# Optimization experiments

Measured on AMD Instinct MI355X. Metric: run time of the kernel, lower is better.

Reference implementation:

```python
import jax, jax.numpy as jnp
import numpy as np

D_MODEL = 1024
N_HEADS = 16
D_HEAD = D_MODEL // N_HEADS  # 64
SCALE = 1.0 / float(np.sqrt(D_HEAD))


def setup_inputs() -> dict:
    key = jax.random.key(0)
    kx, kq, kk, kv, ko = jax.random.split(key, 5)
    B, L = 1, 4096
    x = jax.random.normal(kx, (B, L, D_MODEL), dtype=jnp.float32)
    init = 0.02  # small init so softmax isn't saturated
    Wq = jax.random.normal(kq, (D_MODEL, D_MODEL), dtype=jnp.float32) * init
    Wk = jax.random.normal(kk, (D_MODEL, D_MODEL), dtype=jnp.float32) * init
    Wv = jax.random.normal(kv, (D_MODEL, D_MODEL), dtype=jnp.float32) * init
    Wo = jax.random.normal(ko, (D_MODEL, D_MODEL), dtype=jnp.float32) * init
    return {"x": x, "Wq": Wq, "Wk": Wk, "Wv": Wv, "Wo": Wo}


def reference(x, Wq, Wk, Wv, Wo):
    # x: [B, L, d_model]; torch Linear (no bias): y = x @ W.T
    B, L, _ = x.shape

    def split_heads(t):  # [B, L, d_model] -> [B, H, L, Dh]
        return t.reshape(B, L, N_HEADS, D_HEAD).transpose(0, 2, 1, 3)

    q = split_heads(x @ Wq.T)
    k = split_heads(x @ Wk.T)
    v = split_heads(x @ Wv.T)

    # Full (non-flash) attention: explicit [B, H, L, L] scores (causal=False, eval dropout=0)
    scores = jnp.einsum("bhld,bhmd->bhlm", q, k) * SCALE
    attn = jax.nn.softmax(scores, axis=-1)
    out = jnp.einsum("bhlm,bhmd->bhld", attn, v)

    out = out.transpose(0, 2, 1, 3).reshape(B, L, D_MODEL)
    return out @ Wo.T
```

## Files before the change

kernel.cpp:

```cpp
#include <hip/hip_runtime.h>

typedef _Float16 f16_t;
typedef __fp16 fp16x2 __attribute__((ext_vector_type(2)));
typedef _Float16 f16x2 __attribute__((ext_vector_type(2)));
typedef _Float16 f16x4 __attribute__((ext_vector_type(4)));
typedef _Float16 f16x8 __attribute__((ext_vector_type(8)));
typedef float f32x4 __attribute__((ext_vector_type(4)));

#define D_MODEL 1024
#define LSEQ 4096
#define NH 16
#define DH 64
#define QSCALE 0.18033688011112042f

#define GLDS16(g, l)                                                     \
    __builtin_amdgcn_global_load_lds(                                    \
        (const __attribute__((address_space(1))) void*)(g),              \
        (__attribute__((address_space(3))) void*)(l), 16, 0, 0)

#define WAIT_VM(n) asm volatile("s_waitcnt vmcnt(" #n ")" ::: "memory")

__global__ __launch_bounds__(256) void cvt_x(const float* __restrict__ in,
                                             f16_t* __restrict__ out, int n) {
    int i = (blockIdx.x * 256 + threadIdx.x) * 4;
    if (i + 3 < n) {
        float4 v = *(const float4*)&in[i];
        alignas(8) f16_t o4[4] = {(f16_t)v.x, (f16_t)v.y, (f16_t)v.z, (f16_t)v.w};
        *(uint2*)&out[i] = *(const uint2*)o4;
    }
}

__global__ __launch_bounds__(256) void cvt_w4(const float* __restrict__ w0,
                                              const float* __restrict__ w1,
                                              const float* __restrict__ w2,
                                              const float* __restrict__ w3,
                                              f16_t* __restrict__ out) {
    const int q = blockIdx.y;
    const float* src = (q == 0) ? w0 : (q == 1) ? w1 : (q == 2) ? w2 : w3;
    const float scale = (q == 0) ? QSCALE : 1.f;
    int i = (blockIdx.x * 256 + threadIdx.x) * 4;
    float4 v = *(const float4*)&src[i];
    alignas(8) f16_t o4[4] = {(f16_t)(v.x * scale), (f16_t)(v.y * scale),
                              (f16_t)(v.z * scale), (f16_t)(v.w * scale)};
    *(uint2*)&out[(size_t)q * (D_MODEL * D_MODEL) + i] = *(const uint2*)o4;
}

__global__ __launch_bounds__(256, 3) void gemm_f16(const f16_t* __restrict__ A,
                                                   const f16_t* __restrict__ B,
                                                   void* __restrict__ Cout,
                                                   int M, int N, int K, int mode) {
    __shared__ alignas(16) f16_t As[3][128 * 32];
    __shared__ alignas(16) f16_t Bs[3][128 * 32];

    const int tid  = threadIdx.x;
    const int wave = tid >> 6;
    const int lane = tid & 63;
    const int quad = lane >> 4;
    const int l16  = lane & 15;
    const int wm = (wave & 1) * 64;
    const int wn = (wave >> 1) * 64;
    const int bm = blockIdx.x * 128;
    const int bn = blockIdx.y * 128;

    f32x4 acc[4][4] = {};
    const int nk = K / 32;

    auto stage = [&](int kt, int b) {
        const int c0 = wave * 2;
        GLDS16(&A[(size_t)(bm + c0 * 16 + l16) * K + kt * 32 + quad * 8],
               &As[b][c0 * 512]);
        GLDS16(&A[(size_t)(bm + (c0 + 1) * 16 + l16) * K + kt * 32 + quad * 8],
               &As[b][(c0 + 1) * 512]);
        GLDS16(&B[(size_t)(bn + c0 * 16 + l16) * K + kt * 32 + quad * 8],
               &Bs[b][c0 * 512]);
        GLDS16(&B[(size_t)(bn + (c0 + 1) * 16 + l16) * K + kt * 32 + quad * 8],
               &Bs[b][(c0 + 1) * 512]);
    };

    stage(0, 0);
    stage(1, 1);
    for (int kt = 0; kt < nk; ++kt) {
        const int cb = kt % 3;
        if (kt < nk - 1) WAIT_VM(4);
        else             WAIT_VM(0);
        __syncthreads();
        if (kt + 2 < nk) stage(kt + 2, (kt + 2) % 3);

        f16x8 af[4], bfr[4];
#pragma unroll
        for (int mt = 0; mt < 4; ++mt)
            af[mt] = *(const f16x8*)&As[cb][((wm >> 4) + mt) * 512 + lane * 8];
#pragma unroll
        for (int nt = 0; nt < 4; ++nt)
            bfr[nt] = *(const f16x8*)&Bs[cb][((wn >> 4) + nt) * 512 + lane * 8];
#pragma unroll
        for (int mt = 0; mt < 4; ++mt)
#pragma unroll
            for (int nt = 0; nt < 4; ++nt)
                acc[mt][nt] = __builtin_amdgcn_mfma_f32_16x16x32_f16(
                    bfr[nt], af[mt], acc[mt][nt], 0, 0, 0);
    }

#pragma unroll
    for (int mt = 0; mt < 4; ++mt)
#pragma unroll
        for (int nt = 0; nt < 4; ++nt) {
            int row = bm + wm + mt * 16 + l16;
            int col = bn + wn + nt * 16 + quad * 4;
            if (mode == 0) {
                f16x4 p = {(f16_t)acc[mt][nt][0], (f16_t)acc[mt][nt][1],
                           (f16_t)acc[mt][nt][2], (f16_t)acc[mt][nt][3]};
                *(f16x4*)&((f16_t*)Cout)[((size_t)(col >> 6) * M + row) * 64 +
                                         (col & 63)] = p;
            } else {
                *(f32x4*)&((float*)Cout)[(size_t)row * N + col] = acc[mt][nt];
            }
        }
}

__global__ __launch_bounds__(256) void transpose_v(const f16_t* __restrict__ vh,
                                                   f16_t* __restrict__ v4) {
    __shared__ f16_t Ts[64][72];
    const int t = threadIdx.x;
    const int lt = blockIdx.x;
    const int head = blockIdx.y;

#pragma unroll
    for (int i = 0; i < 2; ++i) {
        int idx = t + i * 256;
        int row = idx >> 3, part = idx & 7;
        *(uint4*)&Ts[row][part * 8] =
            *(const uint4*)&vh[((size_t)head * LSEQ + lt * 64 + row) * DH + part * 8];
    }
    __syncthreads();

    const int c8  = t >> 5;
    const int mtp = c8 >> 2, dt = c8 & 3;
    const int l0  = (t & 31) * 2;
    alignas(16) f16_t buf[16];
#pragma unroll
    for (int li = 0; li < 2; ++li) {
        const int l = l0 + li;
        const int g = l >> 4, l16 = l & 15;
#pragma unroll
        for (int j = 0; j < 8; ++j) {
            int key = mtp * 32 + (j < 4 ? 4 * g + j : 16 + 4 * g + (j - 4));
            buf[li * 8 + j] = Ts[key][dt * 16 + l16];
        }
    }
    f16_t* dst = v4 + (size_t)head * (LSEQ * DH) + (size_t)lt * 4096 + c8 * 512 + l0 * 8;
    *(uint4*)&dst[0] = *(const uint4*)&buf[0];
    *(uint4*)&dst[8] = *(const uint4*)&buf[8];
}

__global__ __launch_bounds__(512, 4) void attn_kernel(const f16_t* __restrict__ qh,
                                                      const f16_t* __restrict__ kh,
                                                      const f16_t* __restrict__ v4,
                                                      f16_t* __restrict__ ao) {
    __shared__ alignas(16) f16_t smem[32768];
    __shared__ alignas(16) float lscr[8 * 64];
    f16_t* KsB = smem;
    f16_t* VsB = smem + 16384;

    const int tid  = threadIdx.x;
    const int wave = tid >> 6;
    const int lane = tid & 63;
    const int quad = lane >> 4;
    const int l16  = lane & 15;
    const int wq   = wave & 3;
    const int kha  = wave >> 2;

    const int id = blockIdx.x;
    const int head = id & 15;
    const int qrow0 = (id >> 4) * 128 + wq * 32;

    const f16_t* Q  = qh + (size_t)head * LSEQ * DH;
    const f16_t* K  = kh + (size_t)head * LSEQ * DH;
    const f16_t* V4 = v4 + (size_t)head * (LSEQ * DH);

    f16x8 qf[2][2];
#pragma unroll
    for (int qt = 0; qt < 2; ++qt)
#pragma unroll
        for (int kc = 0; kc < 2; ++kc)
            qf[qt][kc] = *(const f16x8*)
                &Q[(size_t)(qrow0 + qt * 16 + l16) * DH + kc * 32 + quad * 8];

    f32x4 o[4][2] = {};
    float lp[2] = {0.f, 0.f};

    auto stage = [&](int kt, int b) {
        f16_t* ks = KsB + (kha * 2 + b) * 4096;
        f16_t* vs = VsB + (kha * 2 + b) * 4096;
        const int ktg = kha * 32 + kt;
#pragma unroll
        for (int jj = 0; jj < 2; ++jj) {
            const int j = wq * 2 + jj;
            GLDS16(&K[(size_t)(ktg * 64 + wq * 16 + l16) * DH + jj * 32 + quad * 8],
                   &ks[j * 512]);
            GLDS16(&V4[(size_t)ktg * 4096 + wq * 1024 + jj * 512 + lane * 8],
                   &vs[wq * 1024 + jj * 512]);
        }
    };

    const int NT = LSEQ / 2 / 64;
    stage(0, 0);
    for (int kt = 0; kt < NT; ++kt) {
        const int cb = kt & 1;
        WAIT_VM(0);
        __syncthreads();
        if (kt + 1 < NT) stage(kt + 1, cb ^ 1);

        const f16_t* ks = KsB + (kha * 2 + cb) * 4096;
        const f16_t* vs = VsB + (kha * 2 + cb) * 4096;

#pragma unroll
        for (int mtp = 0; mtp < 2; ++mtp) {
            f32x4 s[2][2] = {};
#pragma unroll
            for (int h = 0; h < 2; ++h) {
                const int mt = mtp * 2 + h;
                f16x8 kf0 = *(const f16x8*)&ks[(mt * 2 + 0) * 512 + lane * 8];
                f16x8 kf1 = *(const f16x8*)&ks[(mt * 2 + 1) * 512 + lane * 8];
#pragma unroll
                for (int qt = 0; qt < 2; ++qt) {
                    s[h][qt] = __builtin_amdgcn_mfma_f32_16x16x32_f16(
                        kf0, qf[qt][0], s[h][qt], 0, 0, 0);
                    s[h][qt] = __builtin_amdgcn_mfma_f32_16x16x32_f16(
                        kf1, qf[qt][1], s[h][qt], 0, 0, 0);
                }
            }

            f16x8 vfd[4];
#pragma unroll
            for (int dt = 0; dt < 4; ++dt)
                vfd[dt] = *(const f16x8*)&vs[(mtp * 4 + dt) * 512 + lane * 8];

#pragma unroll
            for (int qt = 0; qt < 2; ++qt) {
                float e0 = __builtin_amdgcn_exp2f(s[0][qt][0]);
                float e1 = __builtin_amdgcn_exp2f(s[0][qt][1]);
                float e2 = __builtin_amdgcn_exp2f(s[0][qt][2]);
                float e3 = __builtin_amdgcn_exp2f(s[0][qt][3]);
                float e4 = __builtin_amdgcn_exp2f(s[1][qt][0]);
                float e5 = __builtin_amdgcn_exp2f(s[1][qt][1]);
                float e6 = __builtin_amdgcn_exp2f(s[1][qt][2]);
                float e7 = __builtin_amdgcn_exp2f(s[1][qt][3]);
                lp[qt] += ((e0 + e1) + (e2 + e3)) + ((e4 + e5) + (e6 + e7));
                fp16x2 p01 = __builtin_amdgcn_cvt_pkrtz(e0, e1);
                fp16x2 p23 = __builtin_amdgcn_cvt_pkrtz(e2, e3);
                fp16x2 p45 = __builtin_amdgcn_cvt_pkrtz(e4, e5);
                fp16x2 p67 = __builtin_amdgcn_cvt_pkrtz(e6, e7);
                f16x8 p = {__builtin_bit_cast(f16x2, p01)[0],
                           __builtin_bit_cast(f16x2, p01)[1],
                           __builtin_bit_cast(f16x2, p23)[0],
                           __builtin_bit_cast(f16x2, p23)[1],
                           __builtin_bit_cast(f16x2, p45)[0],
                           __builtin_bit_cast(f16x2, p45)[1],
                           __builtin_bit_cast(f16x2, p67)[0],
                           __builtin_bit_cast(f16x2, p67)[1]};
#pragma unroll
                for (int dt = 0; dt < 4; ++dt)
                    o[dt][qt] = __builtin_amdgcn_mfma_f32_16x16x32_f16(
                        vfd[dt], p, o[dt][qt], 0, 0, 0);
            }
        }
    }

    __syncthreads();
    float* scr = (float*)smem;
    if (wave >= 4) {
#pragma unroll
        for (int dt = 0; dt < 4; ++dt)
#pragma unroll
            for (int qt = 0; qt < 2; ++qt)
                *(f32x4*)&scr[(((wave - 4) * 8 + dt * 2 + qt) * 64 + lane) * 4] =
                    o[dt][qt];
#pragma unroll
        for (int qt = 0; qt < 2; ++qt)
            lscr[((wave - 4) * 2 + qt) * 64 + lane] = lp[qt];
    }
    __syncthreads();
    if (wave < 4) {
#pragma unroll
        for (int dt = 0; dt < 4; ++dt)
#pragma unroll
            for (int qt = 0; qt < 2; ++qt)
                o[dt][qt] += *(const f32x4*)
                    &scr[((wave * 8 + dt * 2 + qt) * 64 + lane) * 4];
#pragma unroll
        for (int qt = 0; qt < 2; ++qt) {
            float t = lp[qt] + lscr[(wave * 2 + qt) * 64 + lane];
            t += __shfl_xor(t, 16, 64);
            t += __shfl_xor(t, 32, 64);
            lp[qt] = 1.f / t;
        }
#pragma unroll
        for (int dt = 0; dt < 4; ++dt)
#pragma unroll
            for (int qt = 0; qt < 2; ++qt) {
                f16x4 ov = {(f16_t)(o[dt][qt][0] * lp[qt]),
                            (f16_t)(o[dt][qt][1] * lp[qt]),
                            (f16_t)(o[dt][qt][2] * lp[qt]),
                            (f16_t)(o[dt][qt][3] * lp[qt])};
                int qrow = qrow0 + qt * 16 + l16;
                *(f16x4*)&ao[(size_t)qrow * D_MODEL + head * 64 + dt * 16 +
                             quad * 4] = ov;
            }
    }
}

extern "C" void kernel_launch(void* const* d_in, const int* in_sizes, int n_in,
                              void* d_out, int out_size, void* d_ws, size_t ws_size,
                              hipStream_t stream) {
    const float* x  = (const float*)d_in[0];
    const float* Wq = (const float*)d_in[1];
    const float* Wk = (const float*)d_in[2];
    const float* Wv = (const float*)d_in[3];
    const float* Wo = (const float*)d_in[4];

    f16_t* xb = (f16_t*)d_ws;
    f16_t* wq = xb + (size_t)LSEQ * D_MODEL;
    f16_t* wo = wq + (size_t)3 * D_MODEL * D_MODEL;
    f16_t* qh = wo + (size_t)D_MODEL * D_MODEL;
    f16_t* kh = qh + (size_t)LSEQ * D_MODEL;
    f16_t* vh = kh + (size_t)LSEQ * D_MODEL;
    f16_t* v4 = vh + (size_t)LSEQ * D_MODEL;
    f16_t* ao = v4 + (size_t)LSEQ * D_MODEL;

    const int nx = LSEQ * D_MODEL;
    cvt_x<<<nx / 1024, 256, 0, stream>>>(x, xb, nx);
    cvt_w4<<<dim3(D_MODEL * D_MODEL / 1024, 4), 256, 0, stream>>>(Wq, Wk, Wv, Wo, wq);

    gemm_f16<<<dim3(LSEQ / 128, 3 * D_MODEL / 128), 256, 0, stream>>>(
        xb, wq, qh, LSEQ, 3 * D_MODEL, D_MODEL, 0);

    transpose_v<<<dim3(LSEQ / 64, NH), 256, 0, stream>>>(vh, v4);

    attn_kernel<<<dim3((LSEQ / 128) * NH), 512, 0, stream>>>(qh, kh, v4, ao);

    gemm_f16<<<dim3(LSEQ / 128, D_MODEL / 128), 256, 0, stream>>>(
        ao, wo, d_out, LSEQ, D_MODEL, D_MODEL, 1);
}
```

Baseline: 245.7 us.

## Give each wave 16 query rows over full key range with triple buffering

The attention kernel drops the split-KV scheme, in which two wave groups each covered half the keys for 32 query rows and were merged through LDS at the end. Now each of 8 waves owns 16 query rows and walks the full key sequence. K/V staging becomes a 3-deep ring with a prefetch distance of two tiles, and s_setprio is raised around the MFMA section. This removes the cross-wave reduction and halves the per-wave accumulator registers. In exchange, every block streams all 64 key tiles (twice as many as before), and each K/V tile loaded into LDS is reused by 8 waves instead of 4.

```diff
diff --git a/kernel.cpp b/kernel.cpp
--- a/kernel.cpp
+++ b/kernel.cpp
@@ -157,156 +157,111 @@
                                                       const f16_t* __restrict__ kh,
                                                       const f16_t* __restrict__ v4,
                                                       f16_t* __restrict__ ao) {
-    __shared__ alignas(16) f16_t smem[32768];
-    __shared__ alignas(16) float lscr[8 * 64];
-    f16_t* KsB = smem;
-    f16_t* VsB = smem + 16384;
+    __shared__ alignas(16) f16_t Ks[3][4096];
+    __shared__ alignas(16) f16_t Vs[3][4096];
 
     const int tid  = threadIdx.x;
     const int wave = tid >> 6;
     const int lane = tid & 63;
     const int quad = lane >> 4;
     const int l16  = lane & 15;
-    const int wq   = wave & 3;
-    const int kha  = wave >> 2;
 
     const int id = blockIdx.x;
     const int head = id & 15;
-    const int qrow0 = (id >> 4) * 128 + wq * 32;
-
-    const f16_t* Q  = qh + (size_t)head * LSEQ * DH;
-    const f16_t* K  = kh + (size_t)head * LSEQ * DH;
-    const f16_t* V4 = v4 + (size_t)head * (LSEQ * DH);
-
-    f16x8 qf[2][2];
-#pragma unroll
-    for (int qt = 0; qt < 2; ++qt)
-#pragma unroll
-        for (int kc = 0; kc < 2; ++kc)
-            qf[qt][kc] = *(const f16x8*)
-                &Q[(size_t)(qrow0 + qt * 16 + l16) * DH + kc * 32 + quad * 8];
-
-    f32x4 o[4][2] = {};
-    float lp[2] = {0.f, 0.f};
+    const int qrow0 = (id >> 4) * 128 + wave * 16;
+
+    const f16_t* Q   = qh + (size_t)head * LSEQ * DH;
+    const f16_t* K   = kh + (size_t)head * LSEQ * DH;
+    const f16_t* V4h = v4 + (size_t)head * LSEQ * DH;
+
+    f16x8 qf[2];
+#pragma unroll
+    for (int kc = 0; kc < 2; ++kc)
+        qf[kc] = *(const f16x8*)
+            &Q[(size_t)(qrow0 + l16) * DH + kc * 32 + quad * 8];
+
+    f32x4 o[4] = {};
+    float lp = 0.f;
 
     auto stage = [&](int kt, int b) {
-        f16_t* ks = KsB + (kha * 2 + b) * 4096;
-        f16_t* vs = VsB + (kha * 2 + b) * 4096;
-        const int ktg = kha * 32 + kt;
-#pragma unroll
-        for (int jj = 0; jj < 2; ++jj) {
-            const int j = wq * 2 + jj;
-            GLDS16(&K[(size_t)(ktg * 64 + wq * 16 + l16) * DH + jj * 32 + quad * 8],
-                   &ks[j * 512]);
-            GLDS16(&V4[(size_t)ktg * 4096 + wq * 1024 + jj * 512 + lane * 8],
-                   &vs[wq * 1024 + jj * 512]);
-        }
+        const int c = wave;
+        GLDS16(&K[(size_t)(kt * 64 + (c >> 1) * 16 + l16) * DH + (c & 1) * 32 + quad * 8],
+               &Ks[b][c * 512]);
+        GLDS16(&V4h[(size_t)kt * 4096 + c * 512 + lane * 8],
+               &Vs[b][c * 512]);
     };
 
-    const int NT = LSEQ / 2 / 64;
     stage(0, 0);
+    stage(1, 1);
+
+    const int NT = LSEQ / 64;
     for (int kt = 0; kt < NT; ++kt) {
-        const int cb = kt & 1;
-        WAIT_VM(0);
+        const int cb = kt % 3;
+        if (kt < NT - 1) WAIT_VM(2);
+        else             WAIT_VM(0);
         __syncthreads();
-        if (kt + 1 < NT) stage(kt + 1, cb ^ 1);
-
-        const f16_t* ks = KsB + (kha * 2 + cb) * 4096;
-        const f16_t* vs = VsB + (kha * 2 + cb) * 4096;
-
+        if (kt + 2 < NT) stage(kt + 2, (kt + 2) % 3);
+
+        const f16_t* ks = Ks[cb];
+        const f16_t* vs = Vs[cb];
+
+        __builtin_amdgcn_s_setprio(1);
 #pragma unroll
         for (int mtp = 0; mtp < 2; ++mtp) {
-            f32x4 s[2][2] = {};
+            f32x4 s[2] = {};
 #pragma unroll
             for (int h = 0; h < 2; ++h) {
                 const int mt = mtp * 2 + h;
                 f16x8 kf0 = *(const f16x8*)&ks[(mt * 2 + 0) * 512 + lane * 8];
                 f16x8 kf1 = *(const f16x8*)&ks[(mt * 2 + 1) * 512 + lane * 8];
-#pragma unroll
-                for (int qt = 0; qt < 2; ++qt) {
-                    s[h][qt] = __builtin_amdgcn_mfma_f32_16x16x32_f16(
-                        kf0, qf[qt][0], s[h][qt], 0, 0, 0);
-                    s[h][qt] = __builtin_amdgcn_mfma_f32_16x16x32_f16(
-                        kf1, qf[qt][1], s[h][qt], 0, 0, 0);
-                }
+                s[h] = __builtin_amdgcn_mfma_f32_16x16x32_f16(kf0, qf[0],
+                                                              s[h], 0, 0, 0);
+                s[h] = __builtin_amdgcn_mfma_f32_16x16x32_f16(kf1, qf[1],
+                                                              s[h], 0, 0, 0);
             }
 
-            f16x8 vfd[4];
-#pragma unroll
-            for (int dt = 0; dt < 4; ++dt)
-                vfd[dt] = *(const f16x8*)&vs[(mtp * 4 + dt) * 512 + lane * 8];
-
-#pragma unroll
-            for (int qt = 0; qt < 2; ++qt) {
-                float e0 = __builtin_amdgcn_exp2f(s[0][qt][0]);
-                float e1 = __builtin_amdgcn_exp2f(s[0][qt][1]);
-                float e2 = __builtin_amdgcn_exp2f(s[0][qt][2]);
-                float e3 = __builtin_amdgcn_exp2f(s[0][qt][3]);
-                float e4 = __builtin_amdgcn_exp2f(s[1][qt][0]);
-                float e5 = __builtin_amdgcn_exp2f(s[1][qt][1]);
-                float e6 = __builtin_amdgcn_exp2f(s[1][qt][2]);
-                float e7 = __builtin_amdgcn_exp2f(s[1][qt][3]);
-                lp[qt] += ((e0 + e1) + (e2 + e3)) + ((e4 + e5) + (e6 + e7));
-                fp16x2 p01 = __builtin_amdgcn_cvt_pkrtz(e0, e1);
-                fp16x2 p23 = __builtin_amdgcn_cvt_pkrtz(e2, e3);
-                fp16x2 p45 = __builtin_amdgcn_cvt_pkrtz(e4, e5);
-                fp16x2 p67 = __builtin_amdgcn_cvt_pkrtz(e6, e7);
-                f16x8 p = {__builtin_bit_cast(f16x2, p01)[0],
-                           __builtin_bit_cast(f16x2, p01)[1],
-                           __builtin_bit_cast(f16x2, p23)[0],
-                           __builtin_bit_cast(f16x2, p23)[1],
-                           __builtin_bit_cast(f16x2, p45)[0],
-                           __builtin_bit_cast(f16x2, p45)[1],
-                           __builtin_bit_cast(f16x2, p67)[0],
-                           __builtin_bit_cast(f16x2, p67)[1]};
-#pragma unroll
-                for (int dt = 0; dt < 4; ++dt)
-                    o[dt][qt] = __builtin_amdgcn_mfma_f32_16x16x32_f16(
-                        vfd[dt], p, o[dt][qt], 0, 0, 0);
+            float e0 = __builtin_amdgcn_exp2f(s[0][0]);
+            float e1 = __builtin_amdgcn_exp2f(s[0][1]);
+            float e2 = __builtin_amdgcn_exp2f(s[0][2]);
+            float e3 = __builtin_amdgcn_exp2f(s[0][3]);
+            float e4 = __builtin_amdgcn_exp2f(s[1][0]);
+            float e5 = __builtin_amdgcn_exp2f(s[1][1]);
+            float e6 = __builtin_amdgcn_exp2f(s[1][2]);
+            float e7 = __builtin_amdgcn_exp2f(s[1][3]);
+            lp += ((e0 + e1) + (e2 + e3)) + ((e4 + e5) + (e6 + e7));
+            fp16x2 p01 = __builtin_amdgcn_cvt_pkrtz(e0, e1);
+            fp16x2 p23 = __builtin_amdgcn_cvt_pkrtz(e2, e3);
+            fp16x2 p45 = __builtin_amdgcn_cvt_pkrtz(e4, e5);
+            fp16x2 p67 = __builtin_amdgcn_cvt_pkrtz(e6, e7);
+            f16x8 p = {__builtin_bit_cast(f16x2, p01)[0],
+                       __builtin_bit_cast(f16x2, p01)[1],
+                       __builtin_bit_cast(f16x2, p23)[0],
+                       __builtin_bit_cast(f16x2, p23)[1],
+                       __builtin_bit_cast(f16x2, p45)[0],
+                       __builtin_bit_cast(f16x2, p45)[1],
+                       __builtin_bit_cast(f16x2, p67)[0],
+                       __builtin_bit_cast(f16x2, p67)[1]};
+
+#pragma unroll
+            for (int dt = 0; dt < 4; ++dt) {
+                f16x8 vfd = *(const f16x8*)&vs[(mtp * 4 + dt) * 512 + lane * 8];
+                o[dt] = __builtin_amdgcn_mfma_f32_16x16x32_f16(vfd, p,
+                                                               o[dt], 0, 0, 0);
             }
         }
-    }
-
-    __syncthreads();
-    float* scr = (float*)smem;
-    if (wave >= 4) {
-#pragma unroll
-        for (int dt = 0; dt < 4; ++dt)
-#pragma unroll
-            for (int qt = 0; qt < 2; ++qt)
-                *(f32x4*)&scr[(((wave - 4) * 8 + dt * 2 + qt) * 64 + lane) * 4] =
-                    o[dt][qt];
-#pragma unroll
-        for (int qt = 0; qt < 2; ++qt)
-            lscr[((wave - 4) * 2 + qt) * 64 + lane] = lp[qt];
-    }
-    __syncthreads();
-    if (wave < 4) {
-#pragma unroll
-        for (int dt = 0; dt < 4; ++dt)
-#pragma unroll
-            for (int qt = 0; qt < 2; ++qt)
-                o[dt][qt] += *(const f32x4*)
-                    &scr[((wave * 8 + dt * 2 + qt) * 64 + lane) * 4];
-#pragma unroll
-        for (int qt = 0; qt < 2; ++qt) {
-            float t = lp[qt] + lscr[(wave * 2 + qt) * 64 + lane];
-            t += __shfl_xor(t, 16, 64);
-            t += __shfl_xor(t, 32, 64);
-            lp[qt] = 1.f / t;
-        }
-#pragma unroll
-        for (int dt = 0; dt < 4; ++dt)
-#pragma unroll
-            for (int qt = 0; qt < 2; ++qt) {
-                f16x4 ov = {(f16_t)(o[dt][qt][0] * lp[qt]),
-                            (f16_t)(o[dt][qt][1] * lp[qt]),
-                            (f16_t)(o[dt][qt][2] * lp[qt]),
-                            (f16_t)(o[dt][qt][3] * lp[qt])};
-                int qrow = qrow0 + qt * 16 + l16;
-                *(f16x4*)&ao[(size_t)qrow * D_MODEL + head * 64 + dt * 16 +
-                             quad * 4] = ov;
-            }
+        __builtin_amdgcn_s_setprio(0);
+    }
+
+    float t = lp;
+    t += __shfl_xor(t, 16, 64);
+    t += __shfl_xor(t, 32, 64);
+    const float r = 1.f / t;
+#pragma unroll
+    for (int dt = 0; dt < 4; ++dt) {
+        f16x4 ov = {(f16_t)(o[dt][0] * r), (f16_t)(o[dt][1] * r),
+                    (f16_t)(o[dt][2] * r), (f16_t)(o[dt][3] * r)};
+        *(f16x4*)&ao[(size_t)(qrow0 + l16) * D_MODEL + head * 64 + dt * 16 +
+                     quad * 4] = ov;
     }
 }
 
```

Result: no change. 247.0 us (+0.5%).
